# Kernel tuning notes

Hardware: AMD Instinct MI355X
Metric: run time of the kernel (lower is better)

Reference implementation:

```python
import jax, jax.numpy as jnp
import numpy as np

N_NODES = 50000
N_EDGES = 800000
IN_C = 128
HID = 64          # hidden_channels
OUT_C = 128


def _glorot(key, shape):
    fan_in, fan_out = shape[1], shape[0]
    lim = (6.0 / (fan_in + fan_out)) ** 0.5
    return jax.random.uniform(key, shape, jnp.float32, -lim, lim)


def setup_inputs() -> dict:
    key = jax.random.key(0)
    ks = jax.random.split(key, 12)
    x = jax.random.normal(ks[0], (N_NODES, IN_C), jnp.float32)
    edge_index = jax.random.randint(ks[1], (2, N_EDGES), 0, N_NODES, jnp.int64)
    # SAGEConv params: lin_l (aggregated neighbors, with bias), lin_r (self, no bias)
    # layer1: 128 -> 128 (hidden*2), layer2: 128 -> 64, layer3: 64 -> 128
    d1, d2, d3 = 2 * HID, HID, OUT_C
    return {
        "x": x,
        "edge_index": edge_index,
        "W1l": _glorot(ks[2], (d1, IN_C)), "b1": jnp.zeros((d1,), jnp.float32), "W1r": _glorot(ks[3], (d1, IN_C)),
        "W2l": _glorot(ks[4], (d2, d1)),  "b2": jnp.zeros((d2,), jnp.float32), "W2r": _glorot(ks[5], (d2, d1)),
        "W3l": _glorot(ks[6], (d3, d2)),  "b3": jnp.zeros((d3,), jnp.float32), "W3r": _glorot(ks[7], (d3, d2)),
    }


def _sage_conv(x, src, dst, Wl, bl, Wr):
    # mean-aggregate source features at destination nodes (PyG SAGEConv, aggr='mean')
    msg = x[src]                                                  # [E, d]
    agg = jax.ops.segment_sum(msg, dst, num_segments=N_NODES)     # [N, d]
    cnt = jax.ops.segment_sum(jnp.ones((src.shape[0],), x.dtype), dst, num_segments=N_NODES)
    mean = agg / jnp.maximum(cnt, 1.0)[:, None]
    return mean @ Wl.T + bl + x @ Wr.T


def reference(x, edge_index, W1l, b1, W1r, W2l, b2, W2r, W3l, b3, W3r):
    src, dst = edge_index[0], edge_index[1]
    h1 = jax.nn.relu(_sage_conv(x, src, dst, W1l, b1, W1r))   # dropout: eval mode -> identity
    h2 = jax.nn.relu(_sage_conv(h1, src, dst, W2l, b2, W2r))
    h3 = jax.nn.relu(_sage_conv(h2, src, dst, W3l, b3, W3r))
    return jnp.concatenate([h1, h2, h3], axis=1)              # torch.hstack
```

## Files before the change

### kernel.cpp

```cpp
#include <hip/hip_runtime.h>
#include <hip/hip_bf16.h>

#define N_NODES 50000
#define N_EDGES 800000

constexpr int NP = 50176;
constexpr int E4 = N_EDGES / 4;
constexpr int E8 = N_EDGES / 8;
constexpr int ATB = (E8 + 255) / 256;
constexpr int PGB = (N_NODES + 63) / 64;
constexpr int WCB2 = (64 * 256 + 128 * 128) / 256;

typedef __attribute__((ext_vector_type(8))) short bf16x8;
typedef __attribute__((ext_vector_type(4))) float f32x4;

__device__ __forceinline__ unsigned short f2bf(float f) {
    unsigned u = __float_as_uint(f);
    u += 0x7FFFu + ((u >> 16) & 1u);
    return (unsigned short)(u >> 16);
}

__device__ __forceinline__ bf16x8 pack8(float4 f0, float4 f1) {
    bf16x8 r;
    r[0] = (short)f2bf(f0.x); r[1] = (short)f2bf(f0.y);
    r[2] = (short)f2bf(f0.z); r[3] = (short)f2bf(f0.w);
    r[4] = (short)f2bf(f1.x); r[5] = (short)f2bf(f1.y);
    r[6] = (short)f2bf(f1.z); r[7] = (short)f2bf(f1.w);
    return r;
}

__global__ void zero_kernel(int* __restrict__ p, int n) {
    int i = blockIdx.x * 256 + threadIdx.x;
    if (i < n) p[i] = 0;
}

__global__ __launch_bounds__(256) void prep_kernel(
        const int* __restrict__ dst, int* __restrict__ cnt, int* __restrict__ pos,
        const float* __restrict__ x,
        const float* __restrict__ W1l, const float* __restrict__ b1,
        const float* __restrict__ W1r,
        const float* __restrict__ W2l, const float* __restrict__ W2r,
        const float* __restrict__ W3l, const float* __restrict__ W3r,
        unsigned short* __restrict__ xlb, unsigned short* __restrict__ s1b,
        unsigned short* __restrict__ Wc2, unsigned short* __restrict__ Wc3) {
    int b = blockIdx.x;
    int tid = threadIdx.x;
    if (b < ATB) {
        int t8 = b * 256 + tid;
        if (t8 < E8) {
            int4 d0 = reinterpret_cast<const int4*>(dst)[t8 * 2];
            int4 d1 = reinterpret_cast<const int4*>(dst)[t8 * 2 + 1];
            int4 p0, p1;
            p0.x = atomicAdd(&cnt[d0.x], 1);
            p0.y = atomicAdd(&cnt[d0.y], 1);
            p0.z = atomicAdd(&cnt[d0.z], 1);
            p0.w = atomicAdd(&cnt[d0.w], 1);
            p1.x = atomicAdd(&cnt[d1.x], 1);
            p1.y = atomicAdd(&cnt[d1.y], 1);
            p1.z = atomicAdd(&cnt[d1.z], 1);
            p1.w = atomicAdd(&cnt[d1.w], 1);
            reinterpret_cast<int4*>(pos)[t8 * 2] = p0;
            reinterpret_cast<int4*>(pos)[t8 * 2 + 1] = p1;
        }
    } else if (b < ATB + PGB) {
        int pb = b - ATB;
        int wave = tid >> 6;
        int lane = tid & 63;
        int arow = lane & 15;
        int kseg = lane >> 4;
        bf16x8 bw[4][4];
        float bias_v[4];
        #pragma unroll
        for (int t = 0; t < 4; ++t) {
            int col = wave * 64 + t * 16 + arow;
            const float* wrow = (col < 128) ? (W1l + (size_t)col * 128)
                                            : (W1r + (size_t)(col - 128) * 128);
            bias_v[t] = (col < 128) ? 0.f : b1[col - 128];
            #pragma unroll
            for (int kk = 0; kk < 4; ++kk) {
                int k = kk * 32 + kseg * 8;
                float4 f0 = *reinterpret_cast<const float4*>(wrow + k);
                float4 f1 = *reinterpret_cast<const float4*>(wrow + k + 4);
                bw[t][kk] = pack8(f0, f1);
            }
        }
        for (int g = 0; g < 4; ++g) {
            int node = pb * 64 + g * 16 + arow;
            int ncl = node < N_NODES ? node : 0;
            bf16x8 a[4];
            #pragma unroll
            for (int kk = 0; kk < 4; ++kk) {
                const float* xr = x + (size_t)ncl * 128 + kk * 32 + kseg * 8;
                float4 f0 = *reinterpret_cast<const float4*>(xr);
                float4 f1 = *reinterpret_cast<const float4*>(xr + 4);
                a[kk] = pack8(f0, f1);
            }
            f32x4 acc0 = {0.f,0.f,0.f,0.f}, acc1 = {0.f,0.f,0.f,0.f};
            f32x4 acc2 = {0.f,0.f,0.f,0.f}, acc3 = {0.f,0.f,0.f,0.f};
            #pragma unroll
            for (int kk = 0; kk < 4; ++kk) {
                acc0 = __builtin_amdgcn_mfma_f32_16x16x32_bf16(a[kk], bw[0][kk], acc0, 0, 0, 0);
                acc1 = __builtin_amdgcn_mfma_f32_16x16x32_bf16(a[kk], bw[1][kk], acc1, 0, 0, 0);
                acc2 = __builtin_amdgcn_mfma_f32_16x16x32_bf16(a[kk], bw[2][kk], acc2, 0, 0, 0);
                acc3 = __builtin_amdgcn_mfma_f32_16x16x32_bf16(a[kk], bw[3][kk], acc3, 0, 0, 0);
            }
            int gn0 = pb * 64 + g * 16 + kseg * 4;
            #pragma unroll
            for (int r = 0; r < 4; ++r) {
                int gn = gn0 + r;
                if (gn < N_NODES) {
                    #pragma unroll
                    for (int t = 0; t < 4; ++t) {
                        int col = wave * 64 + t * 16 + arow;
                        float v = (t == 0 ? acc0[r] : t == 1 ? acc1[r] : t == 2 ? acc2[r] : acc3[r])
                                  + bias_v[t];
                        if (col < 128) xlb[(size_t)gn * 128 + col] = f2bf(v);
                        else           s1b[(size_t)gn * 128 + (col - 128)] = f2bf(v);
                    }
                }
            }
        }
    } else {
        int idx = (b - ATB - PGB) * 256 + tid;
        if (idx < 16384) {
            int nr = idx >> 8, k = idx & 255;
            float v = (k < 128) ? W2l[nr * 128 + k] : W2r[nr * 128 + (k - 128)];
            Wc2[idx] = f2bf(v);
        } else {
            int j = idx - 16384;
            int nr = j >> 7, k = j & 127;
            float v = (k < 64) ? W3l[nr * 64 + k] : W3r[nr * 64 + (k - 64)];
            Wc3[j] = f2bf(v);
        }
    }
}

__global__ void assign_kernel(const int* __restrict__ cnt, int* __restrict__ row_ptr,
                              float* __restrict__ inv_deg, int* __restrict__ total, int n) {
    int i = blockIdx.x * blockDim.x + threadIdx.x;
    int lane = threadIdx.x & 63;
    int v = (i < n) ? cnt[i] : 0;
    int s = v;
    #pragma unroll
    for (int off = 1; off < 64; off <<= 1) {
        int t = __shfl_up(s, off);
        if (lane >= off) s += t;
    }
    int base = 0;
    if (lane == 63) base = atomicAdd(total, s);
    base = __shfl(base, 63);
    if (i < n) {
        row_ptr[i] = base + s - v;
        inv_deg[i] = 1.0f / (float)(v > 1 ? v : 1);
    }
}

__global__ void fill_kernel(const int* __restrict__ src, const int* __restrict__ dst,
                            const int* __restrict__ row_ptr,
                            const int* __restrict__ pos, int* __restrict__ edge_src) {
    int t4 = blockIdx.x * 256 + threadIdx.x;
    if (t4 < E4) {
        int4 s4 = reinterpret_cast<const int4*>(src)[t4];
        int4 d4 = reinterpret_cast<const int4*>(dst)[t4];
        int4 p4 = reinterpret_cast<const int4*>(pos)[t4];
        edge_src[row_ptr[d4.x] + p4.x] = s4.x;
        edge_src[row_ptr[d4.y] + p4.y] = s4.y;
        edge_src[row_ptr[d4.z] + p4.z] = s4.z;
        edge_src[row_ptr[d4.w] + p4.w] = s4.w;
    }
}

template<int D, int MODE>
__global__ __launch_bounds__(256) void agg_kernel(
        const unsigned short* __restrict__ hb,
        const int* __restrict__ row_ptr, const int* __restrict__ cnt,
        const int* __restrict__ edge_src,
        const float* __restrict__ inv_deg,
        unsigned short* __restrict__ meanb,
        const unsigned short* __restrict__ s1b,
        float* __restrict__ outF, unsigned short* __restrict__ h1b, int n) {
    constexpr int LPR = D / 8;
    constexpr int EPW = 64 / LPR;
    int wid = (blockIdx.x * 256 + threadIdx.x) >> 6;
    int lane = threadIdx.x & 63;
    if (wid >= n) return;
    int beg = row_ptr[wid];
    int end = beg + cnt[wid];
    float inv = inv_deg[wid];
    int sub = lane / LPR;
    int li = lane % LPR;

    float acc[8];
    #pragma unroll
    for (int j = 0; j < 8; ++j) acc[j] = 0.f;

    for (int e0 = beg; e0 < end; e0 += 4 * EPW) {
        int ea = e0 + sub;
        int eb = ea + EPW;
        int ec = ea + 2 * EPW;
        int ed = ea + 3 * EPW;
        uint4 v0 = {0u,0u,0u,0u}, v1 = {0u,0u,0u,0u}, v2 = {0u,0u,0u,0u}, v3 = {0u,0u,0u,0u};
        if (ea < end) v0 = *reinterpret_cast<const uint4*>(hb + (size_t)edge_src[ea] * D + li * 8);
        if (eb < end) v1 = *reinterpret_cast<const uint4*>(hb + (size_t)edge_src[eb] * D + li * 8);
        if (ec < end) v2 = *reinterpret_cast<const uint4*>(hb + (size_t)edge_src[ec] * D + li * 8);
        if (ed < end) v3 = *reinterpret_cast<const uint4*>(hb + (size_t)edge_src[ed] * D + li * 8);
        unsigned w;
        #define ACCW(u, j0) w = (u); acc[j0] += __uint_as_float(w << 16); acc[j0+1] += __uint_as_float(w & 0xFFFF0000u)
        ACCW(v0.x, 0); ACCW(v0.y, 2); ACCW(v0.z, 4); ACCW(v0.w, 6);
        ACCW(v1.x, 0); ACCW(v1.y, 2); ACCW(v1.z, 4); ACCW(v1.w, 6);
        ACCW(v2.x, 0); ACCW(v2.y, 2); ACCW(v2.z, 4); ACCW(v2.w, 6);
        ACCW(v3.x, 0); ACCW(v3.y, 2); ACCW(v3.z, 4); ACCW(v3.w, 6);
        #undef ACCW
    }
    #pragma unroll
    for (int off = LPR; off < 64; off <<= 1) {
        #pragma unroll
        for (int j = 0; j < 8; ++j) acc[j] += __shfl_xor(acc[j], off);
    }
    if (lane < LPR) {
        if constexpr (MODE == 0) {
            uint4 w;
            w.x = (unsigned)f2bf(acc[0] * inv) | ((unsigned)f2bf(acc[1] * inv) << 16);
            w.y = (unsigned)f2bf(acc[2] * inv) | ((unsigned)f2bf(acc[3] * inv) << 16);
            w.z = (unsigned)f2bf(acc[4] * inv) | ((unsigned)f2bf(acc[5] * inv) << 16);
            w.w = (unsigned)f2bf(acc[6] * inv) | ((unsigned)f2bf(acc[7] * inv) << 16);
            *reinterpret_cast<uint4*>(meanb + (size_t)wid * D + li * 8) = w;
        } else {
            uint4 s4 = *reinterpret_cast<const uint4*>(s1b + (size_t)wid * 128 + li * 8);
            float v[8];
            v[0] = fmaxf(acc[0] * inv + __uint_as_float(s4.x << 16), 0.f);
            v[1] = fmaxf(acc[1] * inv + __uint_as_float(s4.x & 0xFFFF0000u), 0.f);
            v[2] = fmaxf(acc[2] * inv + __uint_as_float(s4.y << 16), 0.f);
            v[3] = fmaxf(acc[3] * inv + __uint_as_float(s4.y & 0xFFFF0000u), 0.f);
            v[4] = fmaxf(acc[4] * inv + __uint_as_float(s4.z << 16), 0.f);
            v[5] = fmaxf(acc[5] * inv + __uint_as_float(s4.z & 0xFFFF0000u), 0.f);
            v[6] = fmaxf(acc[6] * inv + __uint_as_float(s4.w << 16), 0.f);
            v[7] = fmaxf(acc[7] * inv + __uint_as_float(s4.w & 0xFFFF0000u), 0.f);
            float4 r0 = {v[0], v[1], v[2], v[3]};
            float4 r1 = {v[4], v[5], v[6], v[7]};
            float* op = outF + (size_t)wid * 320 + li * 8;
            *reinterpret_cast<float4*>(op) = r0;
            *reinterpret_cast<float4*>(op + 4) = r1;
            uint4 w;
            w.x = (unsigned)f2bf(v[0]) | ((unsigned)f2bf(v[1]) << 16);
            w.y = (unsigned)f2bf(v[2]) | ((unsigned)f2bf(v[3]) << 16);
            w.z = (unsigned)f2bf(v[4]) | ((unsigned)f2bf(v[5]) << 16);
            w.w = (unsigned)f2bf(v[6]) | ((unsigned)f2bf(v[7]) << 16);
            *reinterpret_cast<uint4*>(h1b + (size_t)wid * 128 + li * 8) = w;
        }
    }
}

template<int K, int DOUT, bool WB>
__global__ __launch_bounds__(256, 3) void mfma_gemm_kernel(
        const unsigned short* __restrict__ Ab,
        const unsigned short* __restrict__ Fb,
        const unsigned short* __restrict__ Wc,
        const float* __restrict__ bias,
        float* __restrict__ out, int outs,
        unsigned short* __restrict__ outb, int n) {
    constexpr int DIN = K / 2;
    constexpr int KK = K / 32;
    constexpr int NWC = DOUT / 32;
    constexpr int NWM = 4 / NWC;
    constexpr int GW = 4;
    constexpr int BM = 16 * GW * NWM;
    int wave = threadIdx.x >> 6;
    int lane = threadIdx.x & 63;
    int wc = wave % NWC;
    int wm = wave / NWC;
    int arow = lane & 15;
    int kseg = lane >> 4;

    bf16x8 b0[KK], b1[KK];
    {
        const unsigned short* wp0 = Wc + (size_t)(wc * 32 + arow) * K + kseg * 8;
        const unsigned short* wp1 = wp0 + (size_t)16 * K;
        #pragma unroll
        for (int kk = 0; kk < KK; ++kk) {
            b0[kk] = *reinterpret_cast<const bf16x8*>(wp0 + kk * 32);
            b1[kk] = *reinterpret_cast<const bf16x8*>(wp1 + kk * 32);
        }
    }
    float bv0 = bias[wc * 32 + arow];
    float bv1 = bias[wc * 32 + 16 + arow];

    int g0 = blockIdx.x * (BM / 16) + wm * GW;

    bf16x8 a0[KK], a1[KK];

    #define LOADA(g, dst)                                                          \
    {                                                                              \
        int node = (g0 + (g)) * 16 + arow;                                         \
        int ncl = node < n ? node : 0;                                             \
        _Pragma("unroll")                                                          \
        for (int kk = 0; kk < KK; ++kk) {                                          \
            int k = kk * 32 + kseg * 8;                                            \
            const unsigned short* p = (k < DIN) ? (Ab + (size_t)ncl * DIN + k)     \
                                                : (Fb + (size_t)ncl * DIN + (k - DIN)); \
            dst[kk] = *reinterpret_cast<const bf16x8*>(p);                         \
        }                                                                          \
    }

    #define COMPUTE(g, ab)                                                         \
    {                                                                              \
        f32x4 acc0 = {0.f, 0.f, 0.f, 0.f}, acc1 = {0.f, 0.f, 0.f, 0.f};           \
        _Pragma("unroll")                                                          \
        for (int kk = 0; kk < KK; ++kk) {                                          \
            acc0 = __builtin_amdgcn_mfma_f32_16x16x32_bf16(ab[kk], b0[kk], acc0, 0, 0, 0); \
            acc1 = __builtin_amdgcn_mfma_f32_16x16x32_bf16(ab[kk], b1[kk], acc1, 0, 0, 0); \
        }                                                                          \
        int gbase = (g0 + (g)) * 16 + kseg * 4;                                    \
        _Pragma("unroll")                                                          \
        for (int r = 0; r < 4; ++r) {                                              \
            int gn = gbase + r;                                                    \
            if (gn < n) {                                                          \
                int col0 = wc * 32 + arow;                                         \
                float v0 = fmaxf(acc0[r] + bv0, 0.f);                              \
                float v1 = fmaxf(acc1[r] + bv1, 0.f);                              \
                out[(size_t)gn * outs + col0] = v0;                                \
                out[(size_t)gn * outs + col0 + 16] = v1;                           \
                if constexpr (WB) {                                                \
                    outb[(size_t)gn * DOUT + col0] = f2bf(v0);                     \
                    outb[(size_t)gn * DOUT + col0 + 16] = f2bf(v1);                \
                }                                                                  \
            }                                                                      \
        }                                                                          \
    }

    LOADA(0, a0);
    #pragma unroll
    for (int gp = 0; gp < GW; gp += 2) {
        LOADA(gp + 1, a1);
        COMPUTE(gp, a0);
        if (gp + 2 < GW) LOADA(gp + 2, a0);
        COMPUTE(gp + 1, a1);
    }
    #undef LOADA
    #undef COMPUTE
}

extern "C" void kernel_launch(void* const* d_in, const int* in_sizes, int n_in,
                              void* d_out, int out_size, void* d_ws, size_t ws_size,
                              hipStream_t stream) {
    const float* x   = (const float*)d_in[0];
    const int*   ei  = (const int*)d_in[1];
    const float* W1l = (const float*)d_in[2];
    const float* b1  = (const float*)d_in[3];
    const float* W1r = (const float*)d_in[4];
    const float* W2l = (const float*)d_in[5];
    const float* b2  = (const float*)d_in[6];
    const float* W2r = (const float*)d_in[7];
    const float* W3l = (const float*)d_in[8];
    const float* b3  = (const float*)d_in[9];
    const float* W3r = (const float*)d_in[10];
    float* out = (float*)d_out;

    const int* src = ei;
    const int* dst = ei + N_EDGES;

    int* wsi = (int*)d_ws;
    int*   cnt      = wsi;
    int*   total    = wsi + NP;
    int*   row_ptr  = wsi + NP + 64;
    float* inv_deg  = (float*)(wsi + 2 * NP + 64);
    int*   edge_src = wsi + 3 * NP + 64;
    int*   pos      = edge_src + N_EDGES;
    unsigned short* Wc2 = (unsigned short*)(pos + N_EDGES);
    unsigned short* Wc3 = Wc2 + 64 * 256;
    unsigned short* meanb = Wc3 + 128 * 128;
    unsigned short* xlb = meanb + (size_t)N_NODES * 128;
    unsigned short* s1b = xlb + (size_t)N_NODES * 128;
    unsigned short* h1b = s1b + (size_t)N_NODES * 128;
    unsigned short* h2b = h1b + (size_t)N_NODES * 128;

    zero_kernel<<<(NP + 64 + 255) / 256, 256, 0, stream>>>(cnt, NP + 64);

    prep_kernel<<<ATB + PGB + WCB2, 256, 0, stream>>>(dst, cnt, pos, x,
        W1l, b1, W1r, W2l, W2r, W3l, W3r, xlb, s1b, Wc2, Wc3);

    assign_kernel<<<NP / 256, 256, 0, stream>>>(cnt, row_ptr, inv_deg, total, N_NODES);
    fill_kernel<<<(E4 + 255) / 256, 256, 0, stream>>>(src, dst, row_ptr, pos, edge_src);

    const int AGG_BLOCKS = (N_NODES + 3) / 4;
    const int GB128 = (N_NODES + 127) / 128;
    const int GB64  = (N_NODES + 63) / 64;

    agg_kernel<128, 1><<<AGG_BLOCKS, 256, 0, stream>>>(xlb, row_ptr, cnt, edge_src,
        inv_deg, nullptr, s1b, out, h1b, N_NODES);

    agg_kernel<128, 0><<<AGG_BLOCKS, 256, 0, stream>>>(h1b, row_ptr, cnt, edge_src,
        inv_deg, meanb, nullptr, nullptr, nullptr, N_NODES);
    mfma_gemm_kernel<256, 64, true><<<GB128, 256, 0, stream>>>(meanb, h1b, Wc2, b2,
        out + 128, 320, h2b, N_NODES);

    agg_kernel<64, 0><<<AGG_BLOCKS, 256, 0, stream>>>(h2b, row_ptr, cnt, edge_src,
        inv_deg, meanb, nullptr, nullptr, nullptr, N_NODES);
    mfma_gemm_kernel<128, 128, false><<<GB64, 256, 0, stream>>>(meanb, h2b, Wc3, b3,
        out + 192, 320, nullptr, N_NODES);
}
```

Baseline: 222.0 us.

## Fuse neighbor aggregation with GEMM for layers 2-3 and retile layer-1 prep GEMM

Layers 2 and 3 now use one kernel per layer: each wave computes mean aggregates for 16 nodes into shared memory, and the block then runs the bf16 MFMA GEMM on them together with the self features. This drops the global mean buffer round-trip and two kernel launches. The layer-1 prep GEMM is restructured so each wave handles a single 16-column tile over 2048 nodes across 100 blocks, which lowers register use but re-reads x once per column group and reduces parallelism.

```diff
diff --git a/kernel.cpp b/kernel.cpp
--- a/kernel.cpp
+++ b/kernel.cpp
@@ -8,7 +8,7 @@
 constexpr int E4 = N_EDGES / 4;
 constexpr int E8 = N_EDGES / 8;
 constexpr int ATB = (E8 + 255) / 256;
-constexpr int PGB = (N_NODES + 63) / 64;
+constexpr int PGB = 100;
 constexpr int WCB2 = (64 * 256 + 128 * 128) / 256;
 
 typedef __attribute__((ext_vector_type(8))) short bf16x8;
@@ -34,7 +34,7 @@
     if (i < n) p[i] = 0;
 }
 
-__global__ __launch_bounds__(256) void prep_kernel(
+__global__ __launch_bounds__(256, 8) void prep_kernel(
         const int* __restrict__ dst, int* __restrict__ cnt, int* __restrict__ pos,
         const float* __restrict__ x,
         const float* __restrict__ W1l, const float* __restrict__ b1,
@@ -64,28 +64,24 @@
         }
     } else if (b < ATB + PGB) {
         int pb = b - ATB;
-        int wave = tid >> 6;
-        int lane = tid & 63;
-        int arow = lane & 15;
-        int kseg = lane >> 4;
-        bf16x8 bw[4][4];
-        float bias_v[4];
-        #pragma unroll
-        for (int t = 0; t < 4; ++t) {
-            int col = wave * 64 + t * 16 + arow;
-            const float* wrow = (col < 128) ? (W1l + (size_t)col * 128)
-                                            : (W1r + (size_t)(col - 128) * 128);
-            bias_v[t] = (col < 128) ? 0.f : b1[col - 128];
-            #pragma unroll
-            for (int kk = 0; kk < 4; ++kk) {
-                int k = kk * 32 + kseg * 8;
-                float4 f0 = *reinterpret_cast<const float4*>(wrow + k);
-                float4 f1 = *reinterpret_cast<const float4*>(wrow + k + 4);
-                bw[t][kk] = pack8(f0, f1);
-            }
-        }
-        for (int g = 0; g < 4; ++g) {
-            int node = pb * 64 + g * 16 + arow;
+        int cg = pb & 3;
+        int nc0 = (pb >> 2) * 2048;
+        int wave = tid >> 6, lane = tid & 63;
+        int arow = lane & 15, kseg = lane >> 4;
+        int col = cg * 64 + wave * 16 + arow;
+        const float* wrow = (col < 128) ? (W1l + (size_t)col * 128)
+                                        : (W1r + (size_t)(col - 128) * 128);
+        bf16x8 bw[4];
+        #pragma unroll
+        for (int kk = 0; kk < 4; ++kk) {
+            float4 f0 = *reinterpret_cast<const float4*>(wrow + kk * 32 + kseg * 8);
+            float4 f1 = *reinterpret_cast<const float4*>(wrow + kk * 32 + kseg * 8 + 4);
+            bw[kk] = pack8(f0, f1);
+        }
+        float bias_v = (col < 128) ? 0.f : b1[col - 128];
+        unsigned short* outp = (col < 128) ? (xlb + col) : (s1b + (col - 128));
+        for (int it = 0; it < 128; ++it) {
+            int node = nc0 + it * 16 + arow;
             int ncl = node < N_NODES ? node : 0;
             bf16x8 a[4];
             #pragma unroll
@@ -95,29 +91,15 @@
                 float4 f1 = *reinterpret_cast<const float4*>(xr + 4);
                 a[kk] = pack8(f0, f1);
             }
-            f32x4 acc0 = {0.f,0.f,0.f,0.f}, acc1 = {0.f,0.f,0.f,0.f};
-            f32x4 acc2 = {0.f,0.f,0.f,0.f}, acc3 = {0.f,0.f,0.f,0.f};
-            #pragma unroll
-            for (int kk = 0; kk < 4; ++kk) {
-                acc0 = __builtin_amdgcn_mfma_f32_16x16x32_bf16(a[kk], bw[0][kk], acc0, 0, 0, 0);
-                acc1 = __builtin_amdgcn_mfma_f32_16x16x32_bf16(a[kk], bw[1][kk], acc1, 0, 0, 0);
-                acc2 = __builtin_amdgcn_mfma_f32_16x16x32_bf16(a[kk], bw[2][kk], acc2, 0, 0, 0);
-                acc3 = __builtin_amdgcn_mfma_f32_16x16x32_bf16(a[kk], bw[3][kk], acc3, 0, 0, 0);
-            }
-            int gn0 = pb * 64 + g * 16 + kseg * 4;
+            f32x4 acc = {0.f, 0.f, 0.f, 0.f};
+            #pragma unroll
+            for (int kk = 0; kk < 4; ++kk)
+                acc = __builtin_amdgcn_mfma_f32_16x16x32_bf16(a[kk], bw[kk], acc, 0, 0, 0);
+            int gn0 = nc0 + it * 16 + kseg * 4;
             #pragma unroll
             for (int r = 0; r < 4; ++r) {
                 int gn = gn0 + r;
-                if (gn < N_NODES) {
-                    #pragma unroll
-                    for (int t = 0; t < 4; ++t) {
-                        int col = wave * 64 + t * 16 + arow;
-                        float v = (t == 0 ? acc0[r] : t == 1 ? acc1[r] : t == 2 ? acc2[r] : acc3[r])
-                                  + bias_v[t];
-                        if (col < 128) xlb[(size_t)gn * 128 + col] = f2bf(v);
-                        else           s1b[(size_t)gn * 128 + (col - 128)] = f2bf(v);
-                    }
-                }
+                if (gn < N_NODES) outp[(size_t)gn * 128] = f2bf(acc[r] + bias_v);
             }
         }
     } else {
@@ -170,40 +152,31 @@
     }
 }
 
-template<int D, int MODE>
-__global__ __launch_bounds__(256) void agg_kernel(
+__global__ __launch_bounds__(256) void agg1_kernel(
         const unsigned short* __restrict__ hb,
         const int* __restrict__ row_ptr, const int* __restrict__ cnt,
-        const int* __restrict__ edge_src,
-        const float* __restrict__ inv_deg,
-        unsigned short* __restrict__ meanb,
+        const int* __restrict__ edge_src, const float* __restrict__ inv_deg,
         const unsigned short* __restrict__ s1b,
         float* __restrict__ outF, unsigned short* __restrict__ h1b, int n) {
-    constexpr int LPR = D / 8;
-    constexpr int EPW = 64 / LPR;
+    constexpr int LPR = 16, EPW = 4;
     int wid = (blockIdx.x * 256 + threadIdx.x) >> 6;
     int lane = threadIdx.x & 63;
     if (wid >= n) return;
     int beg = row_ptr[wid];
     int end = beg + cnt[wid];
     float inv = inv_deg[wid];
-    int sub = lane / LPR;
-    int li = lane % LPR;
+    int sub = lane / LPR, li = lane % LPR;
 
     float acc[8];
     #pragma unroll
     for (int j = 0; j < 8; ++j) acc[j] = 0.f;
-
     for (int e0 = beg; e0 < end; e0 += 4 * EPW) {
-        int ea = e0 + sub;
-        int eb = ea + EPW;
-        int ec = ea + 2 * EPW;
-        int ed = ea + 3 * EPW;
+        int ea = e0 + sub, eb = ea + EPW, ec = ea + 2 * EPW, ed = ea + 3 * EPW;
         uint4 v0 = {0u,0u,0u,0u}, v1 = {0u,0u,0u,0u}, v2 = {0u,0u,0u,0u}, v3 = {0u,0u,0u,0u};
-        if (ea < end) v0 = *reinterpret_cast<const uint4*>(hb + (size_t)edge_src[ea] * D + li * 8);
-        if (eb < end) v1 = *reinterpret_cast<const uint4*>(hb + (size_t)edge_src[eb] * D + li * 8);
-        if (ec < end) v2 = *reinterpret_cast<const uint4*>(hb + (size_t)edge_src[ec] * D + li * 8);
-        if (ed < end) v3 = *reinterpret_cast<const uint4*>(hb + (size_t)edge_src[ed] * D + li * 8);
+        if (ea < end) v0 = *reinterpret_cast<const uint4*>(hb + (size_t)edge_src[ea] * 128 + li * 8);
+        if (eb < end) v1 = *reinterpret_cast<const uint4*>(hb + (size_t)edge_src[eb] * 128 + li * 8);
+        if (ec < end) v2 = *reinterpret_cast<const uint4*>(hb + (size_t)edge_src[ec] * 128 + li * 8);
+        if (ed < end) v3 = *reinterpret_cast<const uint4*>(hb + (size_t)edge_src[ed] * 128 + li * 8);
         unsigned w;
         #define ACCW(u, j0) w = (u); acc[j0] += __uint_as_float(w << 16); acc[j0+1] += __uint_as_float(w & 0xFFFF0000u)
         ACCW(v0.x, 0); ACCW(v0.y, 2); ACCW(v0.z, 4); ACCW(v0.w, 6);
@@ -218,126 +191,147 @@
         for (int j = 0; j < 8; ++j) acc[j] += __shfl_xor(acc[j], off);
     }
     if (lane < LPR) {
-        if constexpr (MODE == 0) {
-            uint4 w;
-            w.x = (unsigned)f2bf(acc[0] * inv) | ((unsigned)f2bf(acc[1] * inv) << 16);
-            w.y = (unsigned)f2bf(acc[2] * inv) | ((unsigned)f2bf(acc[3] * inv) << 16);
-            w.z = (unsigned)f2bf(acc[4] * inv) | ((unsigned)f2bf(acc[5] * inv) << 16);
-            w.w = (unsigned)f2bf(acc[6] * inv) | ((unsigned)f2bf(acc[7] * inv) << 16);
-            *reinterpret_cast<uint4*>(meanb + (size_t)wid * D + li * 8) = w;
-        } else {
-            uint4 s4 = *reinterpret_cast<const uint4*>(s1b + (size_t)wid * 128 + li * 8);
-            float v[8];
-            v[0] = fmaxf(acc[0] * inv + __uint_as_float(s4.x << 16), 0.f);
-            v[1] = fmaxf(acc[1] * inv + __uint_as_float(s4.x & 0xFFFF0000u), 0.f);
-            v[2] = fmaxf(acc[2] * inv + __uint_as_float(s4.y << 16), 0.f);
-            v[3] = fmaxf(acc[3] * inv + __uint_as_float(s4.y & 0xFFFF0000u), 0.f);
-            v[4] = fmaxf(acc[4] * inv + __uint_as_float(s4.z << 16), 0.f);
-            v[5] = fmaxf(acc[5] * inv + __uint_as_float(s4.z & 0xFFFF0000u), 0.f);
-            v[6] = fmaxf(acc[6] * inv + __uint_as_float(s4.w << 16), 0.f);
-            v[7] = fmaxf(acc[7] * inv + __uint_as_float(s4.w & 0xFFFF0000u), 0.f);
-            float4 r0 = {v[0], v[1], v[2], v[3]};
-            float4 r1 = {v[4], v[5], v[6], v[7]};
-            float* op = outF + (size_t)wid * 320 + li * 8;
-            *reinterpret_cast<float4*>(op) = r0;
-            *reinterpret_cast<float4*>(op + 4) = r1;
-            uint4 w;
-            w.x = (unsigned)f2bf(v[0]) | ((unsigned)f2bf(v[1]) << 16);
-            w.y = (unsigned)f2bf(v[2]) | ((unsigned)f2bf(v[3]) << 16);
-            w.z = (unsigned)f2bf(v[4]) | ((unsigned)f2bf(v[5]) << 16);
-            w.w = (unsigned)f2bf(v[6]) | ((unsigned)f2bf(v[7]) << 16);
-            *reinterpret_cast<uint4*>(h1b + (size_t)wid * 128 + li * 8) = w;
-        }
+        uint4 s4 = *reinterpret_cast<const uint4*>(s1b + (size_t)wid * 128 + li * 8);
+        float v[8];
+        v[0] = fmaxf(acc[0] * inv + __uint_as_float(s4.x << 16), 0.f);
+        v[1] = fmaxf(acc[1] * inv + __uint_as_float(s4.x & 0xFFFF0000u), 0.f);
+        v[2] = fmaxf(acc[2] * inv + __uint_as_float(s4.y << 16), 0.f);
+        v[3] = fmaxf(acc[3] * inv + __uint_as_float(s4.y & 0xFFFF0000u), 0.f);
+        v[4] = fmaxf(acc[4] * inv + __uint_as_float(s4.z << 16), 0.f);
+        v[5] = fmaxf(acc[5] * inv + __uint_as_float(s4.z & 0xFFFF0000u), 0.f);
+        v[6] = fmaxf(acc[6] * inv + __uint_as_float(s4.w << 16), 0.f);
+        v[7] = fmaxf(acc[7] * inv + __uint_as_float(s4.w & 0xFFFF0000u), 0.f);
+        float4 r0 = {v[0], v[1], v[2], v[3]};
+        float4 r1 = {v[4], v[5], v[6], v[7]};
+        float* op = outF + (size_t)wid * 320 + li * 8;
+        *reinterpret_cast<float4*>(op) = r0;
+        *reinterpret_cast<float4*>(op + 4) = r1;
+        uint4 w;
+        w.x = (unsigned)f2bf(v[0]) | ((unsigned)f2bf(v[1]) << 16);
+        w.y = (unsigned)f2bf(v[2]) | ((unsigned)f2bf(v[3]) << 16);
+        w.z = (unsigned)f2bf(v[4]) | ((unsigned)f2bf(v[5]) << 16);
+        w.w = (unsigned)f2bf(v[6]) | ((unsigned)f2bf(v[7]) << 16);
+        *reinterpret_cast<uint4*>(h1b + (size_t)wid * 128 + li * 8) = w;
     }
 }
 
 template<int K, int DOUT, bool WB>
-__global__ __launch_bounds__(256, 3) void mfma_gemm_kernel(
-        const unsigned short* __restrict__ Ab,
+__global__ __launch_bounds__(256, 4) void fused_kernel(
         const unsigned short* __restrict__ Fb,
+        const int* __restrict__ row_ptr, const int* __restrict__ cnt,
+        const int* __restrict__ edge_src, const float* __restrict__ inv_deg,
         const unsigned short* __restrict__ Wc,
         const float* __restrict__ bias,
         float* __restrict__ out, int outs,
         unsigned short* __restrict__ outb, int n) {
     constexpr int DIN = K / 2;
     constexpr int KK = K / 32;
-    constexpr int NWC = DOUT / 32;
-    constexpr int NWM = 4 / NWC;
-    constexpr int GW = 4;
-    constexpr int BM = 16 * GW * NWM;
-    int wave = threadIdx.x >> 6;
-    int lane = threadIdx.x & 63;
-    int wc = wave % NWC;
-    int wm = wave / NWC;
-    int arow = lane & 15;
-    int kseg = lane >> 4;
-
-    bf16x8 b0[KK], b1[KK];
+    constexpr int KKD = DIN / 32;
+    constexpr int TPW = DOUT / 64;
+    constexpr int LPR = DIN / 8;
+    constexpr int EPW = 64 / LPR;
+    constexpr int LROW = 152;
+    __shared__ unsigned short meanL[64 * LROW];
+
+    int tid = threadIdx.x;
+    int wave = tid >> 6, lane = tid & 63;
+    int nb0 = blockIdx.x * 64;
+
     {
-        const unsigned short* wp0 = Wc + (size_t)(wc * 32 + arow) * K + kseg * 8;
-        const unsigned short* wp1 = wp0 + (size_t)16 * K;
+        int sub = lane / LPR, li = lane % LPR;
+        for (int nl = 0; nl < 16; ++nl) {
+            int node = nb0 + wave * 16 + nl;
+            if (node >= n) break;
+            int beg = row_ptr[node];
+            int end = beg + cnt[node];
+            float inv = inv_deg[node];
+            float acc[8];
+            #pragma unroll
+            for (int j = 0; j < 8; ++j) acc[j] = 0.f;
+            for (int e0 = beg; e0 < end; e0 += 4 * EPW) {
+                int ea = e0 + sub, eb = ea + EPW, ec = ea + 2 * EPW, ed = ea + 3 * EPW;
+                uint4 v0 = {0u,0u,0u,0u}, v1 = {0u,0u,0u,0u}, v2 = {0u,0u,0u,0u}, v3 = {0u,0u,0u,0u};
+                if (ea < end) v0 = *reinterpret_cast<const uint4*>(Fb + (size_t)edge_src[ea] * DIN + li * 8);
+                if (eb < end) v1 = *reinterpret_cast<const uint4*>(Fb + (size_t)edge_src[eb] * DIN + li * 8);
+                if (ec < end) v2 = *reinterpret_cast<const uint4*>(Fb + (size_t)edge_src[ec] * DIN + li * 8);
+                if (ed < end) v3 = *reinterpret_cast<const uint4*>(Fb + (size_t)edge_src[ed] * DIN + li * 8);
+                unsigned w;
+                #define ACCW(u, j0) w = (u); acc[j0] += __uint_as_float(w << 16); acc[j0+1] += __uint_as_float(w & 0xFFFF0000u)
+                ACCW(v0.x, 0); ACCW(v0.y, 2); ACCW(v0.z, 4); ACCW(v0.w, 6);
+                ACCW(v1.x, 0); ACCW(v1.y, 2); ACCW(v1.z, 4); ACCW(v1.w, 6);
+                ACCW(v2.x, 0); ACCW(v2.y, 2); ACCW(v2.z, 4); ACCW(v2.w, 6);
+                ACCW(v3.x, 0); ACCW(v3.y, 2); ACCW(v3.z, 4); ACCW(v3.w, 6);
+                #undef ACCW
+            }
+            #pragma unroll
+            for (int off = LPR; off < 64; off <<= 1) {
+                #pragma unroll
+                for (int j = 0; j < 8; ++j) acc[j] += __shfl_xor(acc[j], off);
+            }
+            if (lane < LPR) {
+                uint4 w;
+                w.x = (unsigned)f2bf(acc[0] * inv) | ((unsigned)f2bf(acc[1] * inv) << 16);
+                w.y = (unsigned)f2bf(acc[2] * inv) | ((unsigned)f2bf(acc[3] * inv) << 16);
+                w.z = (unsigned)f2bf(acc[4] * inv) | ((unsigned)f2bf(acc[5] * inv) << 16);
+                w.w = (unsigned)f2bf(acc[6] * inv) | ((unsigned)f2bf(acc[7] * inv) << 16);
+                *reinterpret_cast<uint4*>(&meanL[(wave * 16 + nl) * LROW + li * 8]) = w;
+            }
+        }
+    }
+    __syncthreads();
+
+    int arow = lane & 15, kseg = lane >> 4;
+    bf16x8 b0[KK], b1[TPW == 2 ? KK : 1];
+    float bv0, bv1 = 0.f;
+    {
+        const unsigned short* wp0 = Wc + (size_t)(wave * 16 * TPW + arow) * K + kseg * 8;
+        #pragma unroll
+        for (int kk = 0; kk < KK; ++kk)
+            b0[kk] = *reinterpret_cast<const bf16x8*>(wp0 + kk * 32);
+        bv0 = bias[wave * 16 * TPW + arow];
+        if constexpr (TPW == 2) {
+            const unsigned short* wp1 = wp0 + (size_t)16 * K;
+            #pragma unroll
+            for (int kk = 0; kk < KK; ++kk)
+                b1[kk] = *reinterpret_cast<const bf16x8*>(wp1 + kk * 32);
+            bv1 = bias[wave * 16 * TPW + 16 + arow];
+        }
+    }
+    #pragma unroll
+    for (int g = 0; g < 4; ++g) {
+        int node = nb0 + g * 16 + arow;
+        int ncl = node < n ? node : 0;
+        bf16x8 a[KK];
+        #pragma unroll
+        for (int kk = 0; kk < KKD; ++kk)
+            a[kk] = *reinterpret_cast<const bf16x8*>(&meanL[(g * 16 + arow) * LROW + kseg * 8 + kk * 32]);
+        #pragma unroll
+        for (int kk = KKD; kk < KK; ++kk)
+            a[kk] = *reinterpret_cast<const bf16x8*>(Fb + (size_t)ncl * DIN + (kk - KKD) * 32 + kseg * 8);
+        f32x4 acc0 = {0.f,0.f,0.f,0.f}, acc1 = {0.f,0.f,0.f,0.f};
         #pragma unroll
         for (int kk = 0; kk < KK; ++kk) {
-            b0[kk] = *reinterpret_cast<const bf16x8*>(wp0 + kk * 32);
-            b1[kk] = *reinterpret_cast<const bf16x8*>(wp1 + kk * 32);
-        }
-    }
-    float bv0 = bias[wc * 32 + arow];
-    float bv1 = bias[wc * 32 + 16 + arow];
-
-    int g0 = blockIdx.x * (BM / 16) + wm * GW;
-
-    bf16x8 a0[KK], a1[KK];
-
-    #define LOADA(g, dst)                                                          \
-    {                                                                              \
-        int node = (g0 + (g)) * 16 + arow;                                         \
-        int ncl = node < n ? node : 0;                                             \
-        _Pragma("unroll")                                                          \
-        for (int kk = 0; kk < KK; ++kk) {                                          \
-            int k = kk * 32 + kseg * 8;                                            \
-            const unsigned short* p = (k < DIN) ? (Ab + (size_t)ncl * DIN + k)     \
-                                                : (Fb + (size_t)ncl * DIN + (k - DIN)); \
-            dst[kk] = *reinterpret_cast<const bf16x8*>(p);                         \
-        }                                                                          \
-    }
-
-    #define COMPUTE(g, ab)                                                         \
-    {                                                                              \
-        f32x4 acc0 = {0.f, 0.f, 0.f, 0.f}, acc1 = {0.f, 0.f, 0.f, 0.f};           \
-        _Pragma("unroll")                                                          \
-        for (int kk = 0; kk < KK; ++kk) {                                          \
-            acc0 = __builtin_amdgcn_mfma_f32_16x16x32_bf16(ab[kk], b0[kk], acc0, 0, 0, 0); \
-            acc1 = __builtin_amdgcn_mfma_f32_16x16x32_bf16(ab[kk], b1[kk], acc1, 0, 0, 0); \
-        }                                                                          \
-        int gbase = (g0 + (g)) * 16 + kseg * 4;                                    \
-        _Pragma("unroll")                                                          \
-        for (int r = 0; r < 4; ++r) {                                              \
-            int gn = gbase + r;                                                    \
-            if (gn < n) {                                                          \
-                int col0 = wc * 32 + arow;                                         \
-                float v0 = fmaxf(acc0[r] + bv0, 0.f);                              \
-                float v1 = fmaxf(acc1[r] + bv1, 0.f);                              \
-                out[(size_t)gn * outs + col0] = v0;                                \
-                out[(size_t)gn * outs + col0 + 16] = v1;                           \
-                if constexpr (WB) {                                                \
-                    outb[(size_t)gn * DOUT + col0] = f2bf(v0);                     \
-                    outb[(size_t)gn * DOUT + col0 + 16] = f2bf(v1);                \
-                }                                                                  \
-            }                                                                      \
-        }                                                                          \
-    }
-
-    LOADA(0, a0);
-    #pragma unroll
-    for (int gp = 0; gp < GW; gp += 2) {
-        LOADA(gp + 1, a1);
-        COMPUTE(gp, a0);
-        if (gp + 2 < GW) LOADA(gp + 2, a0);
-        COMPUTE(gp + 1, a1);
-    }
-    #undef LOADA
-    #undef COMPUTE
+            acc0 = __builtin_amdgcn_mfma_f32_16x16x32_bf16(a[kk], b0[kk], acc0, 0, 0, 0);
+            if constexpr (TPW == 2)
+                acc1 = __builtin_amdgcn_mfma_f32_16x16x32_bf16(a[kk], b1[TPW == 2 ? kk : 0], acc1, 0, 0, 0);
+        }
+        int gbase = nb0 + g * 16 + kseg * 4;
+        #pragma unroll
+        for (int r = 0; r < 4; ++r) {
+            int gn = gbase + r;
+            if (gn < n) {
+                int col0 = wave * 16 * TPW + arow;
+                float v0 = fmaxf(acc0[r] + bv0, 0.f);
+                out[(size_t)gn * outs + col0] = v0;
+                if constexpr (WB) outb[(size_t)gn * DOUT + col0] = f2bf(v0);
+                if constexpr (TPW == 2) {
+                    float v1 = fmaxf(acc1[r] + bv1, 0.f);
+                    out[(size_t)gn * outs + col0 + 16] = v1;
+                    if constexpr (WB) outb[(size_t)gn * DOUT + col0 + 16] = f2bf(v1);
+                }
+            }
+        }
+    }
 }
 
 extern "C" void kernel_launch(void* const* d_in, const int* in_sizes, int n_in,
@@ -368,8 +362,7 @@
     int*   pos      = edge_src + N_EDGES;
     unsigned short* Wc2 = (unsigned short*)(pos + N_EDGES);
     unsigned short* Wc3 = Wc2 + 64 * 256;
-    unsigned short* meanb = Wc3 + 128 * 128;
-    unsigned short* xlb = meanb + (size_t)N_NODES * 128;
+    unsigned short* xlb = Wc3 + 128 * 128;
     unsigned short* s1b = xlb + (size_t)N_NODES * 128;
     unsigned short* h1b = s1b + (size_t)N_NODES * 128;
     unsigned short* h2b = h1b + (size_t)N_NODES * 128;
@@ -380,22 +373,18 @@
         W1l, b1, W1r, W2l, W2r, W3l, W3r, xlb, s1b, Wc2, Wc3);
 
     assign_kernel<<<NP / 256, 256, 0, stream>>>(cnt, row_ptr, inv_deg, total, N_NODES);
+
     fill_kernel<<<(E4 + 255) / 256, 256, 0, stream>>>(src, dst, row_ptr, pos, edge_src);
 
     const int AGG_BLOCKS = (N_NODES + 3) / 4;
-    const int GB128 = (N_NODES + 127) / 128;
-    const int GB64  = (N_NODES + 63) / 64;
-
-    agg_kernel<128, 1><<<AGG_BLOCKS, 256, 0, stream>>>(xlb, row_ptr, cnt, edge_src,
-        inv_deg, nullptr, s1b, out, h1b, N_NODES);
-
-    agg_kernel<128, 0><<<AGG_BLOCKS, 256, 0, stream>>>(h1b, row_ptr, cnt, edge_src,
-        inv_deg, meanb, nullptr, nullptr, nullptr, N_NODES);
-    mfma_gemm_kernel<256, 64, true><<<GB128, 256, 0, stream>>>(meanb, h1b, Wc2, b2,
-        out + 128, 320, h2b, N_NODES);
-
-    agg_kernel<64, 0><<<AGG_BLOCKS, 256, 0, stream>>>(h2b, row_ptr, cnt, edge_src,
-        inv_deg, meanb, nullptr, nullptr, nullptr, N_NODES);
-    mfma_gemm_kernel<128, 128, false><<<GB64, 256, 0, stream>>>(meanb, h2b, Wc3, b3,
-        out + 192, 320, nullptr, N_NODES);
-}
+    const int FUSE_BLOCKS = (N_NODES + 63) / 64;
+
+    agg1_kernel<<<AGG_BLOCKS, 256, 0, stream>>>(xlb, row_ptr, cnt, edge_src,
+        inv_deg, s1b, out, h1b, N_NODES);
+
+    fused_kernel<256, 64, true><<<FUSE_BLOCKS, 256, 0, stream>>>(h1b, row_ptr, cnt,
+        edge_src, inv_deg, Wc2, b2, out + 128, 320, h2b, N_NODES);
+
+    fused_kernel<128, 128, false><<<FUSE_BLOCKS, 256, 0, stream>>>(h2b, row_ptr, cnt,
+        edge_src, inv_deg, Wc3, b3, out + 192, 320, nullptr, N_NODES);
+}
```

Result: slower. 381.5 us (+71.8%).

## Split layer-1 projection across column groups with LDS-staged bf16 input tile

Applied to the files above, without the earlier changes.

The layer-1 projection in prep_kernel now launches four blocks per 64-node group, each producing 64 of the 256 output columns. Each block converts its x tile to bf16 once into shared memory, instead of every wave reloading and repacking x from global memory. The result is more parallel blocks with fewer registers each (launch bounds 8), at the cost of reading x four times across blocks and adding a barrier. The first aggregation is also split out into a dedicated agg1_kernel, and the MODE template parameter is removed from agg_kernel.

```diff
diff --git a/kernel.cpp b/kernel.cpp
--- a/kernel.cpp
+++ b/kernel.cpp
@@ -8,7 +8,7 @@
 constexpr int E4 = N_EDGES / 4;
 constexpr int E8 = N_EDGES / 8;
 constexpr int ATB = (E8 + 255) / 256;
-constexpr int PGB = (N_NODES + 63) / 64;
+constexpr int PGB = 782 * 4;
 constexpr int WCB2 = (64 * 256 + 128 * 128) / 256;
 
 typedef __attribute__((ext_vector_type(8))) short bf16x8;
@@ -34,7 +34,7 @@
     if (i < n) p[i] = 0;
 }
 
-__global__ __launch_bounds__(256) void prep_kernel(
+__global__ __launch_bounds__(256, 8) void prep_kernel(
         const int* __restrict__ dst, int* __restrict__ cnt, int* __restrict__ pos,
         const float* __restrict__ x,
         const float* __restrict__ W1l, const float* __restrict__ b1,
@@ -43,6 +43,7 @@
         const float* __restrict__ W3l, const float* __restrict__ W3r,
         unsigned short* __restrict__ xlb, unsigned short* __restrict__ s1b,
         unsigned short* __restrict__ Wc2, unsigned short* __restrict__ Wc3) {
+    __shared__ unsigned short Asl[64 * 136];
     int b = blockIdx.x;
     int tid = threadIdx.x;
     if (b < ATB) {
@@ -64,60 +65,59 @@
         }
     } else if (b < ATB + PGB) {
         int pb = b - ATB;
-        int wave = tid >> 6;
-        int lane = tid & 63;
-        int arow = lane & 15;
-        int kseg = lane >> 4;
-        bf16x8 bw[4][4];
-        float bias_v[4];
+        int ng = pb >> 2;
+        int cg = pb & 3;
+        int nb0 = ng * 64;
+        {
+            int r = tid >> 2, q = tid & 3;
+            int node = nb0 + r;
+            int ncl = node < N_NODES ? node : 0;
+            const float4* xp = reinterpret_cast<const float4*>(x + (size_t)ncl * 128 + q * 32);
+            #pragma unroll
+            for (int i = 0; i < 4; ++i) {
+                float4 f0 = xp[2 * i];
+                float4 f1 = xp[2 * i + 1];
+                uint4 w;
+                w.x = (unsigned)f2bf(f0.x) | ((unsigned)f2bf(f0.y) << 16);
+                w.y = (unsigned)f2bf(f0.z) | ((unsigned)f2bf(f0.w) << 16);
+                w.z = (unsigned)f2bf(f1.x) | ((unsigned)f2bf(f1.y) << 16);
+                w.w = (unsigned)f2bf(f1.z) | ((unsigned)f2bf(f1.w) << 16);
+                *reinterpret_cast<uint4*>(&Asl[r * 136 + q * 32 + i * 8]) = w;
+            }
+        }
+        __syncthreads();
+        int wave = tid >> 6, lane = tid & 63;
+        int arow = lane & 15, kseg = lane >> 4;
+        int col = cg * 64 + wave * 16 + arow;
+        const float* wrow = (col < 128) ? (W1l + (size_t)col * 128)
+                                        : (W1r + (size_t)(col - 128) * 128);
+        bf16x8 bw[4];
         #pragma unroll
-        for (int t = 0; t < 4; ++t) {
-            int col = wave * 64 + t * 16 + arow;
-            const float* wrow = (col < 128) ? (W1l + (size_t)col * 128)
-                                            : (W1r + (size_t)(col - 128) * 128);
-            bias_v[t] = (col < 128) ? 0.f : b1[col - 128];
-            #pragma unroll
-            for (int kk = 0; kk < 4; ++kk) {
-                int k = kk * 32 + kseg * 8;
-                float4 f0 = *reinterpret_cast<const float4*>(wrow + k);
-                float4 f1 = *reinterpret_cast<const float4*>(wrow + k + 4);
-                bw[t][kk] = pack8(f0, f1);
-            }
-        }
+        for (int kk = 0; kk < 4; ++kk) {
+            float4 f0 = *reinterpret_cast<const float4*>(wrow + kk * 32 + kseg * 8);
+            float4 f1 = *reinterpret_cast<const float4*>(wrow + kk * 32 + kseg * 8 + 4);
+            bw[kk] = pack8(f0, f1);
+        }
+        float bias_v = (col < 128) ? 0.f : b1[col - 128];
+        unsigned short* outbase = (col < 128) ? xlb : s1b;
+        int ocol = (col < 128) ? col : (col - 128);
+        #pragma unroll
         for (int g = 0; g < 4; ++g) {
-            int node = pb * 64 + g * 16 + arow;
-            int ncl = node < N_NODES ? node : 0;
             bf16x8 a[4];
             #pragma unroll
-            for (int kk = 0; kk < 4; ++kk) {
-                const float* xr = x + (size_t)ncl * 128 + kk * 32 + kseg * 8;
-                float4 f0 = *reinterpret_cast<const float4*>(xr);
-                float4 f1 = *reinterpret_cast<const float4*>(xr + 4);
-                a[kk] = pack8(f0, f1);
-            }
-            f32x4 acc0 = {0.f,0.f,0.f,0.f}, acc1 = {0.f,0.f,0.f,0.f};
-            f32x4 acc2 = {0.f,0.f,0.f,0.f}, acc3 = {0.f,0.f,0.f,0.f};
+            for (int kk = 0; kk < 4; ++kk)
+                a[kk] = *reinterpret_cast<const bf16x8*>(
+                    &Asl[(g * 16 + arow) * 136 + kk * 32 + kseg * 8]);
+            f32x4 acc = {0.f, 0.f, 0.f, 0.f};
             #pragma unroll
-            for (int kk = 0; kk < 4; ++kk) {
-                acc0 = __builtin_amdgcn_mfma_f32_16x16x32_bf16(a[kk], bw[0][kk], acc0, 0, 0, 0);
-                acc1 = __builtin_amdgcn_mfma_f32_16x16x32_bf16(a[kk], bw[1][kk], acc1, 0, 0, 0);
-                acc2 = __builtin_amdgcn_mfma_f32_16x16x32_bf16(a[kk], bw[2][kk], acc2, 0, 0, 0);
-                acc3 = __builtin_amdgcn_mfma_f32_16x16x32_bf16(a[kk], bw[3][kk], acc3, 0, 0, 0);
-            }
-            int gn0 = pb * 64 + g * 16 + kseg * 4;
+            for (int kk = 0; kk < 4; ++kk)
+                acc = __builtin_amdgcn_mfma_f32_16x16x32_bf16(a[kk], bw[kk], acc, 0, 0, 0);
+            int gn0 = nb0 + g * 16 + kseg * 4;
             #pragma unroll
             for (int r = 0; r < 4; ++r) {
                 int gn = gn0 + r;
-                if (gn < N_NODES) {
-                    #pragma unroll
-                    for (int t = 0; t < 4; ++t) {
-                        int col = wave * 64 + t * 16 + arow;
-                        float v = (t == 0 ? acc0[r] : t == 1 ? acc1[r] : t == 2 ? acc2[r] : acc3[r])
-                                  + bias_v[t];
-                        if (col < 128) xlb[(size_t)gn * 128 + col] = f2bf(v);
-                        else           s1b[(size_t)gn * 128 + (col - 128)] = f2bf(v);
-                    }
-                }
+                if (gn < N_NODES)
+                    outbase[(size_t)gn * 128 + ocol] = f2bf(acc[r] + bias_v);
             }
         }
     } else {
@@ -170,15 +170,75 @@
     }
 }
 
-template<int D, int MODE>
+__global__ __launch_bounds__(256) void agg1_kernel(
+        const unsigned short* __restrict__ hb,
+        const int* __restrict__ row_ptr, const int* __restrict__ cnt,
+        const int* __restrict__ edge_src, const float* __restrict__ inv_deg,
+        const unsigned short* __restrict__ s1b,
+        float* __restrict__ outF, unsigned short* __restrict__ h1b, int n) {
+    constexpr int LPR = 16, EPW = 4;
+    int wid = (blockIdx.x * 256 + threadIdx.x) >> 6;
+    int lane = threadIdx.x & 63;
+    if (wid >= n) return;
+    int beg = row_ptr[wid];
+    int end = beg + cnt[wid];
+    float inv = inv_deg[wid];
+    int sub = lane / LPR, li = lane % LPR;
+
+    float acc[8];
+    #pragma unroll
+    for (int j = 0; j < 8; ++j) acc[j] = 0.f;
+    for (int e0 = beg; e0 < end; e0 += 4 * EPW) {
+        int ea = e0 + sub, eb = ea + EPW, ec = ea + 2 * EPW, ed = ea + 3 * EPW;
+        uint4 v0 = {0u,0u,0u,0u}, v1 = {0u,0u,0u,0u}, v2 = {0u,0u,0u,0u}, v3 = {0u,0u,0u,0u};
+        if (ea < end) v0 = *reinterpret_cast<const uint4*>(hb + (size_t)edge_src[ea] * 128 + li * 8);
+        if (eb < end) v1 = *reinterpret_cast<const uint4*>(hb + (size_t)edge_src[eb] * 128 + li * 8);
+        if (ec < end) v2 = *reinterpret_cast<const uint4*>(hb + (size_t)edge_src[ec] * 128 + li * 8);
+        if (ed < end) v3 = *reinterpret_cast<const uint4*>(hb + (size_t)edge_src[ed] * 128 + li * 8);
+        unsigned w;
+        #define ACCW(u, j0) w = (u); acc[j0] += __uint_as_float(w << 16); acc[j0+1] += __uint_as_float(w & 0xFFFF0000u)
+        ACCW(v0.x, 0); ACCW(v0.y, 2); ACCW(v0.z, 4); ACCW(v0.w, 6);
+        ACCW(v1.x, 0); ACCW(v1.y, 2); ACCW(v1.z, 4); ACCW(v1.w, 6);
+        ACCW(v2.x, 0); ACCW(v2.y, 2); ACCW(v2.z, 4); ACCW(v2.w, 6);
+        ACCW(v3.x, 0); ACCW(v3.y, 2); ACCW(v3.z, 4); ACCW(v3.w, 6);
+        #undef ACCW
+    }
+    #pragma unroll
+    for (int off = LPR; off < 64; off <<= 1) {
+        #pragma unroll
+        for (int j = 0; j < 8; ++j) acc[j] += __shfl_xor(acc[j], off);
+    }
+    if (lane < LPR) {
+        uint4 s4 = *reinterpret_cast<const uint4*>(s1b + (size_t)wid * 128 + li * 8);
+        float v[8];
+        v[0] = fmaxf(acc[0] * inv + __uint_as_float(s4.x << 16), 0.f);
+        v[1] = fmaxf(acc[1] * inv + __uint_as_float(s4.x & 0xFFFF0000u), 0.f);
+        v[2] = fmaxf(acc[2] * inv + __uint_as_float(s4.y << 16), 0.f);
+        v[3] = fmaxf(acc[3] * inv + __uint_as_float(s4.y & 0xFFFF0000u), 0.f);
+        v[4] = fmaxf(acc[4] * inv + __uint_as_float(s4.z << 16), 0.f);
+        v[5] = fmaxf(acc[5] * inv + __uint_as_float(s4.z & 0xFFFF0000u), 0.f);
+        v[6] = fmaxf(acc[6] * inv + __uint_as_float(s4.w << 16), 0.f);
+        v[7] = fmaxf(acc[7] * inv + __uint_as_float(s4.w & 0xFFFF0000u), 0.f);
+        float4 r0 = {v[0], v[1], v[2], v[3]};
+        float4 r1 = {v[4], v[5], v[6], v[7]};
+        float* op = outF + (size_t)wid * 320 + li * 8;
+        *reinterpret_cast<float4*>(op) = r0;
+        *reinterpret_cast<float4*>(op + 4) = r1;
+        uint4 w;
+        w.x = (unsigned)f2bf(v[0]) | ((unsigned)f2bf(v[1]) << 16);
+        w.y = (unsigned)f2bf(v[2]) | ((unsigned)f2bf(v[3]) << 16);
+        w.z = (unsigned)f2bf(v[4]) | ((unsigned)f2bf(v[5]) << 16);
+        w.w = (unsigned)f2bf(v[6]) | ((unsigned)f2bf(v[7]) << 16);
+        *reinterpret_cast<uint4*>(h1b + (size_t)wid * 128 + li * 8) = w;
+    }
+}
+
+template<int D>
 __global__ __launch_bounds__(256) void agg_kernel(
         const unsigned short* __restrict__ hb,
         const int* __restrict__ row_ptr, const int* __restrict__ cnt,
         const int* __restrict__ edge_src,
-        const float* __restrict__ inv_deg,
-        unsigned short* __restrict__ meanb,
-        const unsigned short* __restrict__ s1b,
-        float* __restrict__ outF, unsigned short* __restrict__ h1b, int n) {
+        const float* __restrict__ inv_deg, unsigned short* __restrict__ meanb, int n) {
     constexpr int LPR = D / 8;
     constexpr int EPW = 64 / LPR;
     int wid = (blockIdx.x * 256 + threadIdx.x) >> 6;
@@ -218,36 +278,12 @@
         for (int j = 0; j < 8; ++j) acc[j] += __shfl_xor(acc[j], off);
     }
     if (lane < LPR) {
-        if constexpr (MODE == 0) {
-            uint4 w;
-            w.x = (unsigned)f2bf(acc[0] * inv) | ((unsigned)f2bf(acc[1] * inv) << 16);
-            w.y = (unsigned)f2bf(acc[2] * inv) | ((unsigned)f2bf(acc[3] * inv) << 16);
-            w.z = (unsigned)f2bf(acc[4] * inv) | ((unsigned)f2bf(acc[5] * inv) << 16);
-            w.w = (unsigned)f2bf(acc[6] * inv) | ((unsigned)f2bf(acc[7] * inv) << 16);
-            *reinterpret_cast<uint4*>(meanb + (size_t)wid * D + li * 8) = w;
-        } else {
-            uint4 s4 = *reinterpret_cast<const uint4*>(s1b + (size_t)wid * 128 + li * 8);
-            float v[8];
-            v[0] = fmaxf(acc[0] * inv + __uint_as_float(s4.x << 16), 0.f);
-            v[1] = fmaxf(acc[1] * inv + __uint_as_float(s4.x & 0xFFFF0000u), 0.f);
-            v[2] = fmaxf(acc[2] * inv + __uint_as_float(s4.y << 16), 0.f);
-            v[3] = fmaxf(acc[3] * inv + __uint_as_float(s4.y & 0xFFFF0000u), 0.f);
-            v[4] = fmaxf(acc[4] * inv + __uint_as_float(s4.z << 16), 0.f);
-            v[5] = fmaxf(acc[5] * inv + __uint_as_float(s4.z & 0xFFFF0000u), 0.f);
-            v[6] = fmaxf(acc[6] * inv + __uint_as_float(s4.w << 16), 0.f);
-            v[7] = fmaxf(acc[7] * inv + __uint_as_float(s4.w & 0xFFFF0000u), 0.f);
-            float4 r0 = {v[0], v[1], v[2], v[3]};
-            float4 r1 = {v[4], v[5], v[6], v[7]};
-            float* op = outF + (size_t)wid * 320 + li * 8;
-            *reinterpret_cast<float4*>(op) = r0;
-            *reinterpret_cast<float4*>(op + 4) = r1;
-            uint4 w;
-            w.x = (unsigned)f2bf(v[0]) | ((unsigned)f2bf(v[1]) << 16);
-            w.y = (unsigned)f2bf(v[2]) | ((unsigned)f2bf(v[3]) << 16);
-            w.z = (unsigned)f2bf(v[4]) | ((unsigned)f2bf(v[5]) << 16);
-            w.w = (unsigned)f2bf(v[6]) | ((unsigned)f2bf(v[7]) << 16);
-            *reinterpret_cast<uint4*>(h1b + (size_t)wid * 128 + li * 8) = w;
-        }
+        uint4 w;
+        w.x = (unsigned)f2bf(acc[0] * inv) | ((unsigned)f2bf(acc[1] * inv) << 16);
+        w.y = (unsigned)f2bf(acc[2] * inv) | ((unsigned)f2bf(acc[3] * inv) << 16);
+        w.z = (unsigned)f2bf(acc[4] * inv) | ((unsigned)f2bf(acc[5] * inv) << 16);
+        w.w = (unsigned)f2bf(acc[6] * inv) | ((unsigned)f2bf(acc[7] * inv) << 16);
+        *reinterpret_cast<uint4*>(meanb + (size_t)wid * D + li * 8) = w;
     }
 }
 
@@ -386,16 +422,16 @@
     const int GB128 = (N_NODES + 127) / 128;
     const int GB64  = (N_NODES + 63) / 64;
 
-    agg_kernel<128, 1><<<AGG_BLOCKS, 256, 0, stream>>>(xlb, row_ptr, cnt, edge_src,
-        inv_deg, nullptr, s1b, out, h1b, N_NODES);
-
-    agg_kernel<128, 0><<<AGG_BLOCKS, 256, 0, stream>>>(h1b, row_ptr, cnt, edge_src,
-        inv_deg, meanb, nullptr, nullptr, nullptr, N_NODES);
+    agg1_kernel<<<AGG_BLOCKS, 256, 0, stream>>>(xlb, row_ptr, cnt, edge_src,
+        inv_deg, s1b, out, h1b, N_NODES);
+
+    agg_kernel<128><<<AGG_BLOCKS, 256, 0, stream>>>(h1b, row_ptr, cnt, edge_src,
+        inv_deg, meanb, N_NODES);
     mfma_gemm_kernel<256, 64, true><<<GB128, 256, 0, stream>>>(meanb, h1b, Wc2, b2,
         out + 128, 320, h2b, N_NODES);
 
-    agg_kernel<64, 0><<<AGG_BLOCKS, 256, 0, stream>>>(h2b, row_ptr, cnt, edge_src,
-        inv_deg, meanb, nullptr, nullptr, nullptr, N_NODES);
+    agg_kernel<64><<<AGG_BLOCKS, 256, 0, stream>>>(h2b, row_ptr, cnt, edge_src,
+        inv_deg, meanb, N_NODES);
     mfma_gemm_kernel<128, 128, false><<<GB64, 256, 0, stream>>>(meanb, h2b, Wc3, b3,
         out + 192, 320, nullptr, N_NODES);
 }
```

New measurement: 221.4 us. No clear change (-0.3%).
